# Kernel tuning notes

Hardware: AMD Instinct MI355X
Metric: run time of the kernel (lower is better)

Reference implementation:

```python
import jax, jax.numpy as jnp
import numpy as np

SQRT_2_OVER_PI = float(np.sqrt(2.0 / np.pi))

def gelu(x):
    return 0.5 * x * (1.0 + jnp.tanh(SQRT_2_OVER_PI * (x + 0.044715 * x ** 3)))

def layer_norm(x, w, b, eps=1e-5):
    mean = jnp.mean(x, axis=-1, keepdims=True)
    var = jnp.var(x, axis=-1, keepdims=True)
    return (x - mean) / jnp.sqrt(var + eps) * w + b

B, S, D, H = 4, 2048, 768, 12
HD = D // H

def setup_inputs() -> dict:
    key = jax.random.key(0)
    ks = jax.random.split(key, 13)
    sc = lambda fan_in: 1.0 / np.sqrt(fan_in)
    return {
        "x": jax.random.normal(ks[0], (B, S, D), jnp.float32),
        "ln1_w": jnp.ones((D,), jnp.float32),
        "ln1_b": jnp.zeros((D,), jnp.float32),
        "w_attn": jax.random.normal(ks[1], (D, 3 * D), jnp.float32) * sc(D),
        "b_attn": jax.random.normal(ks[2], (3 * D,), jnp.float32) * 0.02,
        "w_proj": jax.random.normal(ks[3], (D, D), jnp.float32) * sc(D),
        "b_proj": jax.random.normal(ks[4], (D,), jnp.float32) * 0.02,
        "ln2_w": jnp.ones((D,), jnp.float32),
        "ln2_b": jnp.zeros((D,), jnp.float32),
        "w_fc": jax.random.normal(ks[5], (D, 4 * D), jnp.float32) * sc(D),
        "b_fc": jax.random.normal(ks[6], (4 * D,), jnp.float32) * 0.02,
        "w_fc_proj": jax.random.normal(ks[7], (4 * D, D), jnp.float32) * sc(4 * D),
        "b_fc_proj": jax.random.normal(ks[8], (D,), jnp.float32) * 0.02,
    }

def reference(x, ln1_w, ln1_b, w_attn, b_attn, w_proj, b_proj,
              ln2_w, ln2_b, w_fc, b_fc, w_fc_proj, b_fc_proj):
    batch, seq, dim = x.shape
    # --- causal self-attention on ln_1(x) ---
    h = layer_norm(x, ln1_w, ln1_b)
    qkv = h @ w_attn + b_attn                       # [B,S,3D]
    q, k, v = jnp.split(qkv, 3, axis=-1)
    qh = q.reshape(batch, seq, H, HD).transpose(0, 2, 1, 3)  # [B,H,S,hd]
    kh = k.reshape(batch, seq, H, HD).transpose(0, 2, 1, 3)
    vh = v.reshape(batch, seq, H, HD).transpose(0, 2, 1, 3)
    scores = jnp.einsum('bhqd,bhkd->bhqk', qh, kh) / np.sqrt(HD)  # [B,H,S,S]
    causal = jnp.tril(jnp.ones((seq, seq), bool))
    scores = jnp.where(causal, scores, -jnp.inf)
    probs = jax.nn.softmax(scores, axis=-1)
    attn = jnp.einsum('bhqk,bhkd->bhqd', probs, vh)  # [B,H,S,hd]
    attn = attn.transpose(0, 2, 1, 3).reshape(batch, seq, dim)
    x = x + attn @ w_proj + b_proj
    # --- MLP on ln_2(x) ---
    h = layer_norm(x, ln2_w, ln2_b)
    h = gelu(h @ w_fc + b_fc)
    x = x + h @ w_fc_proj + b_fc_proj
    return x
```

## Files before the change

### kernel.cpp

```cpp
#include <hip/hip_runtime.h>

typedef __bf16 bf16x8 __attribute__((ext_vector_type(8)));
typedef float f32x4 __attribute__((ext_vector_type(4)));
typedef unsigned short u16;
typedef u16 u16x8 __attribute__((ext_vector_type(8)));
typedef u16 u16x4 __attribute__((ext_vector_type(4)));

#define DEVI static __device__ __forceinline__

DEVI u16 f2bf(float f) {
  unsigned u = __float_as_uint(f);
  u += 0x7FFFu + ((u >> 16) & 1u);
  return (u16)(u >> 16);
}

DEVI void gload_lds16(const void* g, void* l) {
  __builtin_amdgcn_global_load_lds((const __attribute__((address_space(1))) void*)g,
                                   (__attribute__((address_space(3))) void*)l, 16, 0, 0);
}

__global__ __launch_bounds__(256) void k_transpose_w(const float* __restrict__ in,
                                                     u16* __restrict__ out, int R, int C) {
  __shared__ float tile[64][65];
  const int t = threadIdx.x;
  const int c0 = blockIdx.x * 64, r0 = blockIdx.y * 64;
#pragma unroll
  for (int i = 0; i < 4; ++i) {
    int id = t + i * 256;
    int r = id >> 4, c4 = (id & 15) * 4;
    f32x4 v = *(const f32x4*)(in + (size_t)(r0 + r) * C + c0 + c4);
#pragma unroll
    for (int j = 0; j < 4; ++j) tile[r][c4 + j] = v[j];
  }
  __syncthreads();
  const int oc = t >> 2;
  const int rr = (t & 3) * 16;
  u16x8 lo, hi;
#pragma unroll
  for (int j = 0; j < 8; ++j) lo[j] = f2bf(tile[rr + j][oc]);
#pragma unroll
  for (int j = 0; j < 8; ++j) hi[j] = f2bf(tile[rr + 8 + j][oc]);
  u16* dst = out + (size_t)(c0 + oc) * R + r0 + rr;
  *(u16x8*)dst = lo;
  *(u16x8*)(dst + 8) = hi;
}

__global__ __launch_bounds__(256) void k_transpose_v(const u16* __restrict__ qkv,
                                                     u16* __restrict__ vt) {
  __shared__ u16 tile[64][72];
  const int t = threadIdx.x;
  const int bh = blockIdx.y;
  const int b = bh / 12, h = bh % 12;
  const int s0 = blockIdx.x * 64;
  const u16* src = qkv + (size_t)b * 2048 * 2304 + 1536 + h * 64;
#pragma unroll
  for (int i = 0; i < 2; ++i) {
    int id = t + i * 256;
    int r = id >> 3, c8 = (id & 7) * 8;
    *(u16x8*)&tile[r][c8] = *(const u16x8*)(src + (size_t)(s0 + r) * 2304 + c8);
  }
  __syncthreads();
  const int od = t >> 2;
  const int rr = (t & 3) * 16;
  u16x8 lo, hi;
#pragma unroll
  for (int j = 0; j < 8; ++j) lo[j] = tile[rr + j][od];
#pragma unroll
  for (int j = 0; j < 8; ++j) hi[j] = tile[rr + 8 + j][od];
  u16* dst = vt + ((size_t)bh * 64 + od) * 2048 + s0 + rr;
  *(u16x8*)dst = lo;
  *(u16x8*)(dst + 8) = hi;
}

__global__ __launch_bounds__(192) void k_layernorm(const float* __restrict__ x,
                                                   const float* __restrict__ w,
                                                   const float* __restrict__ bvec,
                                                   u16* __restrict__ out) {
  const int row = blockIdx.x, t = threadIdx.x;
  const float* xr = x + (size_t)row * 768;
  f32x4 v = *(const f32x4*)(xr + t * 4);
  float s = v[0] + v[1] + v[2] + v[3];
  float sq = v[0] * v[0] + v[1] * v[1] + v[2] * v[2] + v[3] * v[3];
#pragma unroll
  for (int m = 1; m < 64; m <<= 1) { s += __shfl_xor(s, m); sq += __shfl_xor(sq, m); }
  __shared__ float red[2][3];
  const int wv = t >> 6;
  if ((t & 63) == 0) { red[0][wv] = s; red[1][wv] = sq; }
  __syncthreads();
  s = red[0][0] + red[0][1] + red[0][2];
  sq = red[1][0] + red[1][1] + red[1][2];
  const float mean = s * (1.0f / 768.0f);
  const float var = sq * (1.0f / 768.0f) - mean * mean;
  const float rstd = rsqrtf(var + 1e-5f);
  f32x4 wv4 = *(const f32x4*)(w + t * 4);
  f32x4 bv4 = *(const f32x4*)(bvec + t * 4);
  u16x4 o;
#pragma unroll
  for (int j = 0; j < 4; ++j) o[j] = f2bf((v[j] - mean) * rstd * wv4[j] + bv4[j]);
  *(u16x4*)(out + (size_t)row * 768 + t * 4) = o;
}

#define EPI_QKV 0
#define EPI_RESID 1
#define EPI_GELU 2

template <int EPI>
__global__ __launch_bounds__(256) void k_gemm(const u16* __restrict__ A,
                                              const u16* __restrict__ BT,
                                              const float* __restrict__ bias,
                                              const float* __restrict__ resid,
                                              void* __restrict__ outp,
                                              int M, int N, int K) {
  __shared__ u16 As[128 * 32];
  __shared__ u16 Bs[128 * 32];
  const int t = threadIdx.x;
  const int lane = t & 63, w = t >> 6;
  const int l15 = lane & 15, l4 = lane >> 4;
  const int wr = w >> 1, wc = w & 1;
  const int m0 = blockIdx.y * 128, n0 = blockIdx.x * 128;

  f32x4 acc[4][4] = {};

  for (int kt = 0; kt < K; kt += 32) {
#pragma unroll
    for (int i = 0; i < 2; ++i) {
      int c = w * 128 + i * 64 + lane;
      int m = c >> 2, k16 = (c & 3) * 8;
      gload_lds16(A + (size_t)(m0 + m) * K + kt + k16, As + c * 8);
    }
#pragma unroll
    for (int i = 0; i < 2; ++i) {
      int c = w * 128 + i * 64 + lane;
      int n = c >> 2, k16 = (c & 3) * 8;
      gload_lds16(BT + (size_t)(n0 + n) * K + kt + k16, Bs + c * 8);
    }
    __syncthreads();
    bf16x8 af[4], bfr[4];
#pragma unroll
    for (int f = 0; f < 4; ++f)
      af[f] = *(const bf16x8*)(As + (wr * 64 + f * 16 + l15) * 32 + l4 * 8);
#pragma unroll
    for (int f = 0; f < 4; ++f)
      bfr[f] = *(const bf16x8*)(Bs + (wc * 64 + f * 16 + l15) * 32 + l4 * 8);
#pragma unroll
    for (int fi = 0; fi < 4; ++fi)
#pragma unroll
      for (int fj = 0; fj < 4; ++fj)
        acc[fi][fj] = __builtin_amdgcn_mfma_f32_16x16x32_bf16(af[fi], bfr[fj], acc[fi][fj], 0, 0, 0);
    __syncthreads();
  }

#pragma unroll
  for (int fi = 0; fi < 4; ++fi) {
    const int mbase = m0 + wr * 64 + fi * 16 + l4 * 4;
#pragma unroll
    for (int fj = 0; fj < 4; ++fj) {
      const int n = n0 + wc * 64 + fj * 16 + l15;
      const float bn = bias[n];
#pragma unroll
      for (int r = 0; r < 4; ++r) {
        const size_t idx = (size_t)(mbase + r) * N + n;
        float val = acc[fi][fj][r] + bn;
        if constexpr (EPI == EPI_QKV) {
          ((u16*)outp)[idx] = f2bf(val);
        } else if constexpr (EPI == EPI_RESID) {
          ((float*)outp)[idx] = val + resid[idx];
        } else {
          float g = 0.5f * val * (1.0f + tanhf(0.7978845608028654f * (val + 0.044715f * val * val * val)));
          ((u16*)outp)[idx] = f2bf(g);
        }
      }
    }
  }
}

__global__ __launch_bounds__(256) void k_attn(const u16* __restrict__ qkv,
                                              const u16* __restrict__ vt,
                                              u16* __restrict__ out) {
  __shared__ u16 Ks[64 * 72];
  __shared__ u16 Vs[64 * 72];
  __shared__ u16 Ps[4][16 * 72];
  const int t = threadIdx.x, lane = t & 63, w = t >> 6;
  const int l15 = lane & 15, l4 = lane >> 4;
  const int qt = blockIdx.x, h = blockIdx.y, b = blockIdx.z;
  const int q0 = qt * 64;
  const u16* qbase = qkv + (size_t)b * 2048 * 2304 + h * 64;
  const u16* kbase = qbase + 768;
  const u16* vtb = vt + ((size_t)(b * 12 + h) * 64) * 2048;

  const int qrow = q0 + w * 16 + l15;
  bf16x8 qf0 = *(const bf16x8*)(qbase + (size_t)qrow * 2304 + l4 * 8);
  bf16x8 qf1 = *(const bf16x8*)(qbase + (size_t)qrow * 2304 + 32 + l4 * 8);

  float m_run[4], l_run[4];
  f32x4 o_acc[4] = {};
#pragma unroll
  for (int r = 0; r < 4; ++r) { m_run[r] = -1e30f; l_run[r] = 0.f; }

  for (int kt = 0; kt <= qt; ++kt) {
    const int kv0 = kt * 64;
#pragma unroll
    for (int i = 0; i < 2; ++i) {
      int id = t + i * 256;
      int r = id >> 3, c8 = (id & 7) * 8;
      *(u16x8*)&Ks[r * 72 + c8] = *(const u16x8*)(kbase + (size_t)(kv0 + r) * 2304 + c8);
      *(u16x8*)&Vs[r * 72 + c8] = *(const u16x8*)(vtb + (size_t)r * 2048 + kv0 + c8);
    }
    __syncthreads();

    f32x4 sa[4] = {};
#pragma unroll
    for (int c = 0; c < 4; ++c) {
      bf16x8 kf0 = *(const bf16x8*)(Ks + (c * 16 + l15) * 72 + l4 * 8);
      bf16x8 kf1 = *(const bf16x8*)(Ks + (c * 16 + l15) * 72 + 32 + l4 * 8);
      sa[c] = __builtin_amdgcn_mfma_f32_16x16x32_bf16(qf0, kf0, sa[c], 0, 0, 0);
      sa[c] = __builtin_amdgcn_mfma_f32_16x16x32_bf16(qf1, kf1, sa[c], 0, 0, 0);
    }

    const int qrl = q0 + w * 16 + l4 * 4;
#pragma unroll
    for (int c = 0; c < 4; ++c)
#pragma unroll
      for (int r = 0; r < 4; ++r) {
        float s = sa[c][r] * 0.125f;
        if (kt == qt && (kv0 + c * 16 + l15) > (qrl + r)) s = -1e30f;
        sa[c][r] = s;
      }

    float pm[4];
#pragma unroll
    for (int r = 0; r < 4; ++r)
      pm[r] = fmaxf(fmaxf(sa[0][r], sa[1][r]), fmaxf(sa[2][r], sa[3][r]));
#pragma unroll
    for (int m = 1; m < 16; m <<= 1)
#pragma unroll
      for (int r = 0; r < 4; ++r) pm[r] = fmaxf(pm[r], __shfl_xor(pm[r], m));

    float sc[4];
#pragma unroll
    for (int r = 0; r < 4; ++r) {
      float mn = fmaxf(m_run[r], pm[r]);
      sc[r] = expf(m_run[r] - mn);
      m_run[r] = mn;
    }
    float ls[4] = {0.f, 0.f, 0.f, 0.f};
#pragma unroll
    for (int c = 0; c < 4; ++c)
#pragma unroll
      for (int r = 0; r < 4; ++r) {
        float p = expf(sa[c][r] - m_run[r]);
        sa[c][r] = p;
        ls[r] += p;
      }
#pragma unroll
    for (int m = 1; m < 16; m <<= 1)
#pragma unroll
      for (int r = 0; r < 4; ++r) ls[r] += __shfl_xor(ls[r], m);
#pragma unroll
    for (int r = 0; r < 4; ++r) l_run[r] = l_run[r] * sc[r] + ls[r];
#pragma unroll
    for (int c = 0; c < 4; ++c)
#pragma unroll
      for (int r = 0; r < 4; ++r) o_acc[c][r] *= sc[r];

    u16* pw = &Ps[w][0];
#pragma unroll
    for (int c = 0; c < 4; ++c)
#pragma unroll
      for (int r = 0; r < 4; ++r)
        pw[(l4 * 4 + r) * 72 + c * 16 + l15] = f2bf(sa[c][r]);
    bf16x8 pa0 = *(const bf16x8*)(pw + l15 * 72 + l4 * 8);
    bf16x8 pa1 = *(const bf16x8*)(pw + l15 * 72 + 32 + l4 * 8);

#pragma unroll
    for (int c = 0; c < 4; ++c) {
      bf16x8 vf0 = *(const bf16x8*)(Vs + (c * 16 + l15) * 72 + l4 * 8);
      bf16x8 vf1 = *(const bf16x8*)(Vs + (c * 16 + l15) * 72 + 32 + l4 * 8);
      o_acc[c] = __builtin_amdgcn_mfma_f32_16x16x32_bf16(pa0, vf0, o_acc[c], 0, 0, 0);
      o_acc[c] = __builtin_amdgcn_mfma_f32_16x16x32_bf16(pa1, vf1, o_acc[c], 0, 0, 0);
    }
    __syncthreads();
  }

#pragma unroll
  for (int c = 0; c < 4; ++c)
#pragma unroll
    for (int r = 0; r < 4; ++r) {
      int qr = q0 + w * 16 + l4 * 4 + r;
      float o = o_acc[c][r] / l_run[r];
      out[((size_t)(b * 2048) + qr) * 768 + h * 64 + c * 16 + l15] = f2bf(o);
    }
}

extern "C" void kernel_launch(void* const* d_in, const int* in_sizes, int n_in,
                              void* d_out, int out_size, void* d_ws, size_t ws_size,
                              hipStream_t stream) {
  (void)in_sizes; (void)n_in; (void)out_size; (void)ws_size;
  const float* x      = (const float*)d_in[0];
  const float* ln1_w  = (const float*)d_in[1];
  const float* ln1_b  = (const float*)d_in[2];
  const float* w_attn = (const float*)d_in[3];
  const float* b_attn = (const float*)d_in[4];
  const float* w_proj = (const float*)d_in[5];
  const float* b_proj = (const float*)d_in[6];
  const float* ln2_w  = (const float*)d_in[7];
  const float* ln2_b  = (const float*)d_in[8];
  const float* w_fc   = (const float*)d_in[9];
  const float* b_fc   = (const float*)d_in[10];
  const float* w_fcp  = (const float*)d_in[11];
  const float* b_fcp  = (const float*)d_in[12];
  float* out = (float*)d_out;

  char* ws = (char*)d_ws;
  u16*   wt_attn = (u16*)(ws + 0);
  u16*   wt_proj = (u16*)(ws + 3538944);
  u16*   wt_fc   = (u16*)(ws + 4718592);
  u16*   wt_fcp  = (u16*)(ws + 9437184);
  u16*   h_ln    = (u16*)(ws + 14155776);
  u16*   qkv     = (u16*)(ws + 26738688);
  u16*   vtb     = (u16*)(ws + 64487424);
  u16*   h_gelu  = qkv;
  u16*   attn    = (u16*)(ws + 77070336);
  float* x2      = (float*)(ws + 89653248);

  k_transpose_w<<<dim3(36, 12), 256, 0, stream>>>(w_attn, wt_attn, 768, 2304);
  k_transpose_w<<<dim3(12, 12), 256, 0, stream>>>(w_proj, wt_proj, 768, 768);
  k_transpose_w<<<dim3(48, 12), 256, 0, stream>>>(w_fc, wt_fc, 768, 3072);
  k_transpose_w<<<dim3(12, 48), 256, 0, stream>>>(w_fcp, wt_fcp, 3072, 768);
  k_layernorm<<<8192, 192, 0, stream>>>(x, ln1_w, ln1_b, h_ln);
  k_gemm<EPI_QKV><<<dim3(18, 64), 256, 0, stream>>>(h_ln, wt_attn, b_attn, nullptr, qkv, 8192, 2304, 768);
  k_transpose_v<<<dim3(32, 48), 256, 0, stream>>>(qkv, vtb);
  k_attn<<<dim3(32, 12, 4), 256, 0, stream>>>(qkv, vtb, attn);
  k_gemm<EPI_RESID><<<dim3(6, 64), 256, 0, stream>>>(attn, wt_proj, b_proj, x, x2, 8192, 768, 768);
  k_layernorm<<<8192, 192, 0, stream>>>(x2, ln2_w, ln2_b, h_ln);
  k_gemm<EPI_GELU><<<dim3(24, 64), 256, 0, stream>>>(h_ln, wt_fc, b_fc, nullptr, h_gelu, 8192, 3072, 768);
  k_gemm<EPI_RESID><<<dim3(6, 64), 256, 0, stream>>>(h_gelu, wt_fcp, b_fcp, x2, out, 8192, 768, 3072);
}
```

Measured before the change: 587.1 us.

## Transpose QK^T layout, fold scale into Q, use exp2 with lazy rescaling in attention

The attention kernel pre-scales Q by log2(e)/sqrt(d) and swaps the MFMA operands so that each lane holds one query row's scores. This reduces the row max and sum reductions to two cross-lane shuffles and lets P be stored to shared memory as packed 4-wide vectors. Softmax now uses exp2f, and the running-max rescale of the accumulator only happens when some row's max grows by more than 8 (in log2 units). Risks are extra rounding from scaling Q in bf16 and, under the lazy rescale, probabilities up to 2^8 before bf16 conversion, which is fine in range but changes numerics slightly.

```diff
diff --git a/kernel.cpp b/kernel.cpp
--- a/kernel.cpp
+++ b/kernel.cpp
@@ -13,6 +13,7 @@
   u += 0x7FFFu + ((u >> 16) & 1u);
   return (u16)(u >> 16);
 }
+DEVI float bf2f(u16 u) { return __uint_as_float(((unsigned)u) << 16); }
 
 DEVI void gload_lds16(const void* g, void* l) {
   __builtin_amdgcn_global_load_lds((const __attribute__((address_space(1))) void*)g,
@@ -182,6 +183,7 @@
   __shared__ u16 Ps[4][16 * 72];
   const int t = threadIdx.x, lane = t & 63, w = t >> 6;
   const int l15 = lane & 15, l4 = lane >> 4;
+  const int l44 = l4 * 4;
   const int qt = blockIdx.x, h = blockIdx.y, b = blockIdx.z;
   const int q0 = qt * 64;
   const u16* qbase = qkv + (size_t)b * 2048 * 2304 + h * 64;
@@ -189,13 +191,22 @@
   const u16* vtb = vt + ((size_t)(b * 12 + h) * 64) * 2048;
 
   const int qrow = q0 + w * 16 + l15;
-  bf16x8 qf0 = *(const bf16x8*)(qbase + (size_t)qrow * 2304 + l4 * 8);
-  bf16x8 qf1 = *(const bf16x8*)(qbase + (size_t)qrow * 2304 + 32 + l4 * 8);
-
-  float m_run[4], l_run[4];
+  bf16x8 qf0, qf1;
+  {
+    const float PRE = 0.18033688011112042f;
+    u16x8 r0 = *(const u16x8*)(qbase + (size_t)qrow * 2304 + l4 * 8);
+    u16x8 r1 = *(const u16x8*)(qbase + (size_t)qrow * 2304 + 32 + l4 * 8);
+    u16x8 s0, s1;
+#pragma unroll
+    for (int j = 0; j < 8; ++j) { s0[j] = f2bf(bf2f(r0[j]) * PRE); s1[j] = f2bf(bf2f(r1[j]) * PRE); }
+    qf0 = *(bf16x8*)&s0;
+    qf1 = *(bf16x8*)&s1;
+  }
+
+  float m_run = -1e30f, l_run = 0.f;
   f32x4 o_acc[4] = {};
-#pragma unroll
-  for (int r = 0; r < 4; ++r) { m_run[r] = -1e30f; l_run[r] = 0.f; }
+  u16* pw = &Ps[w][0];
+  const int qq = w * 16 + l15;
 
   for (int kt = 0; kt <= qt; ++kt) {
     const int kv0 = kt * 64;
@@ -213,82 +224,78 @@
     for (int c = 0; c < 4; ++c) {
       bf16x8 kf0 = *(const bf16x8*)(Ks + (c * 16 + l15) * 72 + l4 * 8);
       bf16x8 kf1 = *(const bf16x8*)(Ks + (c * 16 + l15) * 72 + 32 + l4 * 8);
-      sa[c] = __builtin_amdgcn_mfma_f32_16x16x32_bf16(qf0, kf0, sa[c], 0, 0, 0);
-      sa[c] = __builtin_amdgcn_mfma_f32_16x16x32_bf16(qf1, kf1, sa[c], 0, 0, 0);
-    }
-
-    const int qrl = q0 + w * 16 + l4 * 4;
+      sa[c] = __builtin_amdgcn_mfma_f32_16x16x32_bf16(kf0, qf0, sa[c], 0, 0, 0);
+      sa[c] = __builtin_amdgcn_mfma_f32_16x16x32_bf16(kf1, qf1, sa[c], 0, 0, 0);
+    }
+
+    if (kt == qt) {
+#pragma unroll
+      for (int c = 0; c < 4; ++c)
+#pragma unroll
+        for (int r = 0; r < 4; ++r)
+          if (c * 16 + l44 + r > qq) sa[c][r] = -1e30f;
+    }
+
+    float pm = fmaxf(fmaxf(sa[0][0], sa[0][1]), fmaxf(sa[0][2], sa[0][3]));
+#pragma unroll
+    for (int c = 1; c < 4; ++c)
+      pm = fmaxf(pm, fmaxf(fmaxf(sa[c][0], sa[c][1]), fmaxf(sa[c][2], sa[c][3])));
+    pm = fmaxf(pm, __shfl_xor(pm, 16));
+    pm = fmaxf(pm, __shfl_xor(pm, 32));
+
+    if (__any(pm > m_run + 8.0f)) {
+      float mn = fmaxf(m_run, pm);
+      float scq = exp2f(m_run - mn);
+      m_run = mn;
+      l_run *= scq;
+#pragma unroll
+      for (int r = 0; r < 4; ++r) {
+        float s = __shfl(scq, l44 + r);
+#pragma unroll
+        for (int cd = 0; cd < 4; ++cd) o_acc[cd][r] *= s;
+      }
+    }
+
+    float ls = 0.f;
+    u16x4 pk[4];
 #pragma unroll
     for (int c = 0; c < 4; ++c)
 #pragma unroll
       for (int r = 0; r < 4; ++r) {
-        float s = sa[c][r] * 0.125f;
-        if (kt == qt && (kv0 + c * 16 + l15) > (qrl + r)) s = -1e30f;
-        sa[c][r] = s;
+        float p = exp2f(sa[c][r] - m_run);
+        ls += p;
+        pk[c][r] = f2bf(p);
       }
-
-    float pm[4];
-#pragma unroll
-    for (int r = 0; r < 4; ++r)
-      pm[r] = fmaxf(fmaxf(sa[0][r], sa[1][r]), fmaxf(sa[2][r], sa[3][r]));
-#pragma unroll
-    for (int m = 1; m < 16; m <<= 1)
-#pragma unroll
-      for (int r = 0; r < 4; ++r) pm[r] = fmaxf(pm[r], __shfl_xor(pm[r], m));
-
-    float sc[4];
-#pragma unroll
-    for (int r = 0; r < 4; ++r) {
-      float mn = fmaxf(m_run[r], pm[r]);
-      sc[r] = expf(m_run[r] - mn);
-      m_run[r] = mn;
-    }
-    float ls[4] = {0.f, 0.f, 0.f, 0.f};
+    ls += __shfl_xor(ls, 16);
+    ls += __shfl_xor(ls, 32);
+    l_run += ls;
+
 #pragma unroll
     for (int c = 0; c < 4; ++c)
-#pragma unroll
-      for (int r = 0; r < 4; ++r) {
-        float p = expf(sa[c][r] - m_run[r]);
-        sa[c][r] = p;
-        ls[r] += p;
-      }
-#pragma unroll
-    for (int m = 1; m < 16; m <<= 1)
-#pragma unroll
-      for (int r = 0; r < 4; ++r) ls[r] += __shfl_xor(ls[r], m);
-#pragma unroll
-    for (int r = 0; r < 4; ++r) l_run[r] = l_run[r] * sc[r] + ls[r];
-#pragma unroll
-    for (int c = 0; c < 4; ++c)
-#pragma unroll
-      for (int r = 0; r < 4; ++r) o_acc[c][r] *= sc[r];
-
-    u16* pw = &Ps[w][0];
-#pragma unroll
-    for (int c = 0; c < 4; ++c)
-#pragma unroll
-      for (int r = 0; r < 4; ++r)
-        pw[(l4 * 4 + r) * 72 + c * 16 + l15] = f2bf(sa[c][r]);
+      *(u16x4*)(pw + l15 * 72 + c * 16 + l44) = pk[c];
+
     bf16x8 pa0 = *(const bf16x8*)(pw + l15 * 72 + l4 * 8);
     bf16x8 pa1 = *(const bf16x8*)(pw + l15 * 72 + 32 + l4 * 8);
 
 #pragma unroll
-    for (int c = 0; c < 4; ++c) {
-      bf16x8 vf0 = *(const bf16x8*)(Vs + (c * 16 + l15) * 72 + l4 * 8);
-      bf16x8 vf1 = *(const bf16x8*)(Vs + (c * 16 + l15) * 72 + 32 + l4 * 8);
-      o_acc[c] = __builtin_amdgcn_mfma_f32_16x16x32_bf16(pa0, vf0, o_acc[c], 0, 0, 0);
-      o_acc[c] = __builtin_amdgcn_mfma_f32_16x16x32_bf16(pa1, vf1, o_acc[c], 0, 0, 0);
+    for (int cd = 0; cd < 4; ++cd) {
+      bf16x8 vf0 = *(const bf16x8*)(Vs + (cd * 16 + l15) * 72 + l4 * 8);
+      bf16x8 vf1 = *(const bf16x8*)(Vs + (cd * 16 + l15) * 72 + 32 + l4 * 8);
+      o_acc[cd] = __builtin_amdgcn_mfma_f32_16x16x32_bf16(pa0, vf0, o_acc[cd], 0, 0, 0);
+      o_acc[cd] = __builtin_amdgcn_mfma_f32_16x16x32_bf16(pa1, vf1, o_acc[cd], 0, 0, 0);
     }
     __syncthreads();
   }
 
-#pragma unroll
-  for (int c = 0; c < 4; ++c)
+  float lr[4];
+#pragma unroll
+  for (int r = 0; r < 4; ++r) lr[r] = 1.0f / __shfl(l_run, l44 + r);
+#pragma unroll
+  for (int cd = 0; cd < 4; ++cd)
 #pragma unroll
     for (int r = 0; r < 4; ++r) {
-      int qr = q0 + w * 16 + l4 * 4 + r;
-      float o = o_acc[c][r] / l_run[r];
-      out[((size_t)(b * 2048) + qr) * 768 + h * 64 + c * 16 + l15] = f2bf(o);
+      int qr = q0 + w * 16 + l44 + r;
+      out[((size_t)(b * 2048) + qr) * 768 + h * 64 + cd * 16 + l15] = f2bf(o_acc[cd][r] * lr[r]);
     }
 }
 
```

Measured after the change: 486.5 us. 17.1% less time.
